# Performance work log

Hardware: AMD Instinct MI355X
Metric: run time of the kernel (lower is better)

## Reference

```python
import jax, jax.numpy as jnp
import numpy as np
import math

H = 768      # hidden_dim
NH = 12      # nhead
HD = H // NH # head_dim
FF = 4 * H
B, N = 8, 1024


def _layernorm(x, g, b, eps=1e-5):
    m = jnp.mean(x, axis=-1, keepdims=True)
    v = jnp.var(x, axis=-1, keepdims=True)
    return (x - m) * jax.lax.rsqrt(v + eps) * g + b


def setup_inputs() -> dict:
    key = jax.random.key(0)
    ks = jax.random.split(key, 16)
    s = 1.0 / math.sqrt(H)
    inp = {
        'x': jax.random.normal(ks[0], (B, N, H), jnp.float32),
        'attn_bias': jax.random.normal(ks[1], (NH, N, N), jnp.float32),
        'Wq': jax.random.normal(ks[2], (H, H), jnp.float32) * s,
        'bq': jnp.zeros((H,), jnp.float32),
        'Wk': jax.random.normal(ks[3], (H, H), jnp.float32) * s,
        'bk': jnp.zeros((H,), jnp.float32),
        'Wv': jax.random.normal(ks[4], (H, H), jnp.float32) * s,
        'bv': jnp.zeros((H,), jnp.float32),
        'Wo': jax.random.normal(ks[5], (H, H), jnp.float32) * s,
        'bo': jnp.zeros((H,), jnp.float32),
        'g1': jnp.ones((H,), jnp.float32),
        'be1': jnp.zeros((H,), jnp.float32),
        'W1': jax.random.normal(ks[6], (H, FF), jnp.float32) * s,
        'bf1': jnp.zeros((FF,), jnp.float32),
        'W2': jax.random.normal(ks[7], (FF, H), jnp.float32) * (1.0 / math.sqrt(FF)),
        'bf2': jnp.zeros((H,), jnp.float32),
        'g2': jnp.ones((H,), jnp.float32),
        'be2': jnp.zeros((H,), jnp.float32),
    }
    return inp


def reference(x, attn_bias, Wq, bq, Wk, bk, Wv, bv, Wo, bo, g1, be1, W1, bf1, W2, bf2, g2, be2):
    # dropout in eval mode (identity)
    Bc, Nc, C = x.shape
    q = (x @ Wq + bq).reshape(Bc, Nc, NH, HD).transpose(0, 2, 1, 3)  # [B,H,N,D]
    k = (x @ Wk + bk).reshape(Bc, Nc, NH, HD).transpose(0, 2, 1, 3)
    v = (x @ Wv + bv).reshape(Bc, Nc, NH, HD).transpose(0, 2, 1, 3)
    scores = jnp.einsum('bhnd,bhmd->bhnm', q, k) / math.sqrt(HD)
    scores = scores + attn_bias[None]  # bias broadcast over batch
    probs = jax.nn.softmax(scores, axis=-1)
    out = jnp.einsum('bhnm,bhmd->bhnd', probs, v)
    out = out.transpose(0, 2, 1, 3).reshape(Bc, Nc, C)
    out = out @ Wo + bo
    x = _layernorm(x + out, g1, be1)
    h = jax.nn.gelu(x @ W1 + bf1, approximate=False) @ W2 + bf2
    x = _layernorm(x + h, g2, be2)
    return x
```

## Files before the change

### kernel.cpp

```cpp
#include <hip/hip_runtime.h>
#include <math.h>

#define NH 12
#define HD 64
#define SEQ 1024
#define BATCH 8
#define HDIM 768
#define FFDIM 3072
#define MTOT (BATCH*SEQ)

typedef __attribute__((ext_vector_type(8))) short short8;
typedef __attribute__((ext_vector_type(4))) float f32x4;
typedef __attribute__((ext_vector_type(4))) unsigned short ushort4v;

__device__ __forceinline__ unsigned short f2b(float f) {
    union { float f; unsigned u; } v; v.f = f;
    unsigned r = v.u + 0x7fffu + ((v.u >> 16) & 1u);
    return (unsigned short)(r >> 16);
}

__device__ __forceinline__ f32x4 mfma16(short8 a, short8 b, f32x4 c) {
    return __builtin_amdgcn_mfma_f32_16x16x32_bf16(a, b, c, 0, 0, 0);
}

__device__ __forceinline__ void async_copy16(const unsigned short* g, unsigned short* l) {
    __builtin_amdgcn_global_load_lds(
        (const __attribute__((address_space(1))) unsigned int*)(const void*)g,
        (__attribute__((address_space(3))) unsigned int*)(void*)l, 16, 0, 0);
}

__global__ __launch_bounds__(256) void k_cvt(const float* __restrict__ in,
                                             unsigned short* __restrict__ out, int n) {
    int idx = (blockIdx.x * 256 + threadIdx.x) * 4;
    if (idx >= n) return;
    float4 v = *reinterpret_cast<const float4*>(in + idx);
    ushort4v o;
    o[0] = f2b(v.x); o[1] = f2b(v.y); o[2] = f2b(v.z); o[3] = f2b(v.w);
    *reinterpret_cast<ushort4v*>(out + idx) = o;
}

__global__ __launch_bounds__(256) void k_wt4(const float* __restrict__ W0,
                                             const float* __restrict__ W1,
                                             const float* __restrict__ W2,
                                             const float* __restrict__ W3,
                                             unsigned short* __restrict__ WT) {
    __shared__ float t[32][33];
    const float* W = (blockIdx.z == 0) ? W0 : (blockIdx.z == 1) ? W1 :
                     (blockIdx.z == 2) ? W2 : W3;
    unsigned short* dst = WT + (size_t)blockIdx.z * 768 * 768;
    int n0 = blockIdx.x * 32, k0 = blockIdx.y * 32;
    int x = threadIdx.x & 31, y = threadIdx.x >> 5;
#pragma unroll
    for (int i = y; i < 32; i += 8) t[i][x] = W[(size_t)(k0 + i) * 768 + n0 + x];
    __syncthreads();
#pragma unroll
    for (int i = y; i < 32; i += 8) dst[(size_t)(n0 + i) * 768 + k0 + x] = f2b(t[x][i]);
}

__global__ __launch_bounds__(256) void k_wt(const float* __restrict__ W,
                                            unsigned short* __restrict__ WT, int K, int Nn) {
    __shared__ float t[32][33];
    int n0 = blockIdx.x * 32, k0 = blockIdx.y * 32;
    int x = threadIdx.x & 31, y = threadIdx.x >> 5;
#pragma unroll
    for (int i = y; i < 32; i += 8) t[i][x] = W[(size_t)(k0 + i) * Nn + n0 + x];
    __syncthreads();
#pragma unroll
    for (int i = y; i < 32; i += 8) WT[(size_t)(n0 + i) * K + k0 + x] = f2b(t[x][i]);
}

__global__ void k_bias3(const float* __restrict__ a, const float* __restrict__ b,
                        const float* __restrict__ c, float* __restrict__ o) {
    int i = blockIdx.x * 256 + threadIdx.x;
    if (i >= 3 * HDIM) return;
    o[i] = (i < HDIM) ? a[i] : (i < 2 * HDIM ? b[i - HDIM] : c[i - 2 * HDIM]);
}

__global__ __launch_bounds__(256) void k_vtr(const unsigned short* __restrict__ QKV,
                                             unsigned short* __restrict__ VT) {
    __shared__ unsigned short T[64][72];
    int kt = blockIdx.x * 64;
    int bh = blockIdx.y;
    int b = bh / NH, h = bh % NH;
    int tid = threadIdx.x;
#pragma unroll
    for (int it = 0; it < 2; ++it) {
        int idx = tid + it * 256;
        int r = idx >> 3, c8 = (idx & 7) * 8;
        *reinterpret_cast<short8*>(&T[r][c8]) = *reinterpret_cast<const short8*>(
            &QKV[(size_t)(b * SEQ + kt + r) * 2304 + 1536 + h * 64 + c8]);
    }
    __syncthreads();
#pragma unroll
    for (int it = 0; it < 2; ++it) {
        int idx = tid + it * 256;
        int d = idx >> 3, c8 = (idx & 7) * 8;
        short8 o;
#pragma unroll
        for (int j = 0; j < 8; j++) {
            int slot = c8 + j;
            o[j] = (short)T[(slot & 15) * 4 + (slot >> 4)][d];
        }
        *reinterpret_cast<short8*>(&VT[((size_t)bh * 64 + d) * SEQ + kt + c8]) = o;
    }
}

template<int EPI>
__device__ __forceinline__ void epi_store(float v, size_t oi,
                                          unsigned short* outb, float* outf,
                                          const float* resid) {
    if constexpr (EPI == 0) {
        outb[oi] = f2b(v);
    } else if constexpr (EPI == 1) {
        outf[oi] = v + resid[oi];
    } else {
        float g = 0.5f * v * (1.0f + erff(v * 0.70710678118654752f));
        outb[oi] = f2b(g);
    }
}

template<int EPI>
__global__ __launch_bounds__(256) void k_gemm(const unsigned short* __restrict__ A,
                                              const unsigned short* __restrict__ BT,
                                              const float* __restrict__ bias,
                                              const float* __restrict__ resid,
                                              unsigned short* __restrict__ outb,
                                              float* __restrict__ outf,
                                              int Ndim, int Kdim) {
    __shared__ unsigned short As[128 * 64];
    __shared__ unsigned short Bs[128 * 64];
    int tid = threadIdx.x;
    int wid = tid >> 6, lane = tid & 63;
    int wm = wid >> 1, wn = wid & 1;
    int l15 = lane & 15, l16 = lane >> 4;
    int bm = blockIdx.x * 128, bn = blockIdx.y * 128;

    int srow = wid * 8 + (lane >> 3);
    int scol = 8 * ((lane & 7) ^ (lane >> 3));
    const unsigned short* aptr = A + (size_t)(bm + srow) * Kdim + scol;
    const unsigned short* bptr = BT + (size_t)(bn + srow) * Kdim + scol;

    f32x4 acc[4][4] = {};
    const int swz = (l15 & 7) << 3;

    for (int kt = 0; kt < Kdim; kt += 64) {
#pragma unroll
        for (int c = 0; c < 4; c++) {
            async_copy16(aptr + (size_t)c * 32 * Kdim + kt, As + c * 2048 + wid * 512);
            async_copy16(bptr + (size_t)c * 32 * Kdim + kt, Bs + c * 2048 + wid * 512);
        }
        __syncthreads();
#pragma unroll
        for (int kk = 0; kk < 2; kk++) {
            short8 af[4], bfr[4];
            int cidx = (kk * 32 + l16 * 8) ^ swz;
#pragma unroll
            for (int i = 0; i < 4; i++) {
                af[i]  = *reinterpret_cast<const short8*>(&As[(wm * 64 + i * 16 + l15) * 64 + cidx]);
                bfr[i] = *reinterpret_cast<const short8*>(&Bs[(wn * 64 + i * 16 + l15) * 64 + cidx]);
            }
#pragma unroll
            for (int i = 0; i < 4; i++)
#pragma unroll
                for (int j = 0; j < 4; j++)
                    acc[i][j] = mfma16(af[i], bfr[j], acc[i][j]);
        }
        __syncthreads();
    }

#pragma unroll
    for (int i = 0; i < 4; i++)
#pragma unroll
        for (int j = 0; j < 4; j++) {
            int grow0 = bm + wm * 64 + i * 16 + l16 * 4;
            int gcol = bn + wn * 64 + j * 16 + l15;
            float bcol = bias[gcol];
#pragma unroll
            for (int r = 0; r < 4; r++)
                epi_store<EPI>(acc[i][j][r] + bcol, (size_t)(grow0 + r) * Ndim + gcol,
                               outb, outf, resid);
        }
}

__global__ __launch_bounds__(256) void k_attn(const unsigned short* __restrict__ QKV,
                                              const unsigned short* __restrict__ VT,
                                              const float* __restrict__ bias,
                                              unsigned short* __restrict__ out) {
    __shared__ unsigned short Ks[64][72];
    __shared__ unsigned short Vt[64][72];
    __shared__ unsigned short Ps[4][16][72];

    int bh = blockIdx.y;
    int b = bh / NH, h = bh % NH;
    int q0 = blockIdx.x * 64;
    int tid = threadIdx.x, wid = tid >> 6, lane = tid & 63;
    int l15 = lane & 15, l16 = lane >> 4;

    size_t qrow = (size_t)(b * SEQ + q0 + wid * 16 + l15) * 2304 + h * 64;
    short8 qf0 = *reinterpret_cast<const short8*>(&QKV[qrow + l16 * 8]);
    short8 qf1 = *reinterpret_cast<const short8*>(&QKV[qrow + 32 + l16 * 8]);

    const float* brow = bias + (size_t)h * SEQ * SEQ +
                        (size_t)(q0 + wid * 16 + l16 * 4) * SEQ;

    f32x4 o[4] = {};
    float mrow[4], lrow[4];
#pragma unroll
    for (int r = 0; r < 4; r++) { mrow[r] = -1e30f; lrow[r] = 0.0f; }

    for (int kt = 0; kt < SEQ; kt += 64) {
#pragma unroll
        for (int it = 0; it < 2; ++it) {
            int idx = tid + it * 256;
            int r = idx >> 3, c8 = (idx & 7) * 8;
            int pr = (r & 15) * 4 + (r >> 4);
            *reinterpret_cast<short8*>(&Ks[r][c8]) = *reinterpret_cast<const short8*>(
                &QKV[(size_t)(b * SEQ + kt + pr) * 2304 + 768 + h * 64 + c8]);
            *reinterpret_cast<short8*>(&Vt[r][c8]) = *reinterpret_cast<const short8*>(
                &VT[((size_t)bh * 64 + r) * SEQ + kt + c8]);
        }
        __syncthreads();

        f32x4 s[4];
#pragma unroll
        for (int c = 0; c < 4; c++) {
            f32x4 t = {};
            t = mfma16(qf0, *reinterpret_cast<const short8*>(&Ks[c * 16 + l15][l16 * 8]), t);
            t = mfma16(qf1, *reinterpret_cast<const short8*>(&Ks[c * 16 + l15][32 + l16 * 8]), t);
            s[c] = t;
        }
#pragma unroll
        for (int r = 0; r < 4; r++) {
            float4 bv = *reinterpret_cast<const float4*>(&brow[(size_t)r * SEQ + kt + l15 * 4]);
            s[0][r] = s[0][r] * 0.125f + bv.x;
            s[1][r] = s[1][r] * 0.125f + bv.y;
            s[2][r] = s[2][r] * 0.125f + bv.z;
            s[3][r] = s[3][r] * 0.125f + bv.w;
        }
#pragma unroll
        for (int r = 0; r < 4; r++) {
            float mx = fmaxf(fmaxf(s[0][r], s[1][r]), fmaxf(s[2][r], s[3][r]));
#pragma unroll
            for (int off = 1; off < 16; off <<= 1) mx = fmaxf(mx, __shfl_xor(mx, off, 64));
            float mnew = fmaxf(mrow[r], mx);
            float resc = __expf(mrow[r] - mnew);
            mrow[r] = mnew;
            float sum = 0.0f;
#pragma unroll
            for (int c = 0; c < 4; c++) {
                float p = __expf(s[c][r] - mnew);
                s[c][r] = p; sum += p;
            }
#pragma unroll
            for (int off = 1; off < 16; off <<= 1) sum += __shfl_xor(sum, off, 64);
            lrow[r] = lrow[r] * resc + sum;
#pragma unroll
            for (int dc = 0; dc < 4; dc++) o[dc][r] *= resc;
        }
#pragma unroll
        for (int c = 0; c < 4; c++)
#pragma unroll
            for (int r = 0; r < 4; r++)
                Ps[wid][l16 * 4 + r][c * 16 + l15] = f2b(s[c][r]);
#pragma unroll
        for (int dc = 0; dc < 4; dc++) {
            int d = dc * 16 + l15;
#pragma unroll
            for (int kk = 0; kk < 2; kk++) {
                short8 pa = *reinterpret_cast<const short8*>(&Ps[wid][l15][kk * 32 + l16 * 8]);
                short8 vb = *reinterpret_cast<const short8*>(&Vt[d][kk * 32 + l16 * 8]);
                o[dc] = mfma16(pa, vb, o[dc]);
            }
        }
        __syncthreads();
    }

#pragma unroll
    for (int dc = 0; dc < 4; dc++)
#pragma unroll
        for (int r = 0; r < 4; r++) {
            float v = o[dc][r] / lrow[r];
            size_t row = (size_t)(b * SEQ + q0 + wid * 16 + l16 * 4 + r);
            out[row * 768 + h * 64 + dc * 16 + l15] = f2b(v);
        }
}

template<int WB>
__global__ __launch_bounds__(256) void k_ln(const float* __restrict__ in,
                                            const float* __restrict__ gw,
                                            const float* __restrict__ bw,
                                            float* __restrict__ outf,
                                            unsigned short* __restrict__ outb) {
    int row = blockIdx.x, tid = threadIdx.x;
    const float* x = in + (size_t)row * 768;
    float v0 = x[tid], v1 = x[tid + 256], v2 = x[tid + 512];
    float s = v0 + v1 + v2;
    float s2 = v0 * v0 + v1 * v1 + v2 * v2;
#pragma unroll
    for (int off = 32; off; off >>= 1) {
        s += __shfl_down(s, off, 64);
        s2 += __shfl_down(s2, off, 64);
    }
    __shared__ float red[16];
    if ((tid & 63) == 0) { red[tid >> 6] = s; red[8 + (tid >> 6)] = s2; }
    __syncthreads();
    float ssum = red[0] + red[1] + red[2] + red[3];
    float s2sum = red[8] + red[9] + red[10] + red[11];
    float mean = ssum * (1.0f / 768.0f);
    float var = s2sum * (1.0f / 768.0f) - mean * mean;
    float rstd = rsqrtf(var + 1e-5f);
    float* of = outf + (size_t)row * 768;
    unsigned short* ob = outb ? outb + (size_t)row * 768 : nullptr;
    float vv[3] = { v0, v1, v2 };
#pragma unroll
    for (int i = 0; i < 3; i++) {
        int col = tid + i * 256;
        float y = (vv[i] - mean) * rstd * gw[col] + bw[col];
        of[col] = y;
        if constexpr (WB) ob[col] = f2b(y);
    }
}

constexpr size_t OFF_XB    = 0;
constexpr size_t OFF_QKV   = OFF_XB    + 12582912;
constexpr size_t OFF_ATT   = OFF_QKV   + 37748736;
constexpr size_t OFF_WQKVT = OFF_ATT   + 12582912;
constexpr size_t OFF_WOT   = OFF_WQKVT + 3538944;
constexpr size_t OFF_W1T   = OFF_WOT   + 1179648;
constexpr size_t OFF_W2T   = OFF_W1T   + 4718592;
constexpr size_t OFF_BQKV  = OFF_W2T   + 4718592;
constexpr size_t OFF_TMP   = OFF_BQKV  + 9216;
constexpr size_t OFF_X1F   = OFF_TMP   + 25165824;
constexpr size_t OFF_X1B   = OFF_X1F   + 25165824;
constexpr size_t OFF_H     = OFF_X1B   + 12582912;

extern "C" void kernel_launch(void* const* d_in, const int* in_sizes, int n_in,
                              void* d_out, int out_size, void* d_ws, size_t ws_size,
                              hipStream_t stream) {
    const float* x    = (const float*)d_in[0];
    const float* ab   = (const float*)d_in[1];
    const float* Wq   = (const float*)d_in[2];
    const float* bq   = (const float*)d_in[3];
    const float* Wk   = (const float*)d_in[4];
    const float* bk   = (const float*)d_in[5];
    const float* Wv   = (const float*)d_in[6];
    const float* bv   = (const float*)d_in[7];
    const float* Wo   = (const float*)d_in[8];
    const float* bo   = (const float*)d_in[9];
    const float* g1   = (const float*)d_in[10];
    const float* be1  = (const float*)d_in[11];
    const float* W1   = (const float*)d_in[12];
    const float* bf1  = (const float*)d_in[13];
    const float* W2   = (const float*)d_in[14];
    const float* bf2  = (const float*)d_in[15];
    const float* g2   = (const float*)d_in[16];
    const float* be2  = (const float*)d_in[17];

    char* ws = (char*)d_ws;
    unsigned short* xb    = (unsigned short*)(ws + OFF_XB);
    unsigned short* qkv   = (unsigned short*)(ws + OFF_QKV);
    unsigned short* att   = (unsigned short*)(ws + OFF_ATT);
    unsigned short* wqkvt = (unsigned short*)(ws + OFF_WQKVT);
    unsigned short* wot   = (unsigned short*)(ws + OFF_WOT);
    unsigned short* w1t   = (unsigned short*)(ws + OFF_W1T);
    unsigned short* w2t   = (unsigned short*)(ws + OFF_W2T);
    float*          bqkv  = (float*)(ws + OFF_BQKV);
    float*          tmp   = (float*)(ws + OFF_TMP);
    unsigned short* vt    = (unsigned short*)(ws + OFF_TMP);
    float*          x1f   = (float*)(ws + OFF_X1F);
    unsigned short* x1b   = (unsigned short*)(ws + OFF_X1B);
    unsigned short* hb    = (unsigned short*)(ws + OFF_H);
    float*          out   = (float*)d_out;

    k_cvt<<<dim3(MTOT * HDIM / 1024), dim3(256), 0, stream>>>(x, xb, MTOT * HDIM);
    k_wt4<<<dim3(24, 24, 4), dim3(256), 0, stream>>>(Wq, Wk, Wv, Wo, wqkvt);
    k_wt<<<dim3(96, 24), dim3(256), 0, stream>>>(W1, w1t, HDIM, FFDIM);
    k_wt<<<dim3(24, 96), dim3(256), 0, stream>>>(W2, w2t, FFDIM, HDIM);
    k_bias3<<<dim3(9), dim3(256), 0, stream>>>(bq, bk, bv, bqkv);

    k_gemm<0><<<dim3(64, 18), dim3(256), 0, stream>>>(xb, wqkvt, bqkv, nullptr, qkv, nullptr,
                                                      3 * HDIM, HDIM);
    k_vtr<<<dim3(SEQ / 64, BATCH * NH), dim3(256), 0, stream>>>(qkv, vt);
    k_attn<<<dim3(SEQ / 64, BATCH * NH), dim3(256), 0, stream>>>(qkv, vt, ab, att);
    k_gemm<1><<<dim3(64, 6), dim3(256), 0, stream>>>(att, wot, bo, x, nullptr, tmp,
                                                     HDIM, HDIM);
    k_ln<1><<<dim3(MTOT), dim3(256), 0, stream>>>(tmp, g1, be1, x1f, x1b);
    k_gemm<2><<<dim3(64, 24), dim3(256), 0, stream>>>(x1b, w1t, bf1, nullptr, hb, nullptr,
                                                      FFDIM, HDIM);
    k_gemm<1><<<dim3(64, 6), dim3(256), 0, stream>>>(hb, w2t, bf2, x1f, nullptr, tmp,
                                                     HDIM, FFDIM);
    k_ln<0><<<dim3(MTOT), dim3(256), 0, stream>>>(tmp, g2, be2, out, nullptr);
}
```

Before: 495.5 us.

## Transpose attention score tiles and use lazy online-softmax rescaling

Swaps the MFMA operand order so each lane owns one query row of the score tile. This reduces the row max and sum reductions to two cross-group shuffles and lets K and V be loaded without the row permutation. The 1/sqrt(d) scale is folded into the Wq weights and bias during preprocessing. Online-softmax rescaling is skipped while the running max grows by at most 8. Probabilities are packed to bf16 with v_cvt_pk_bf16 and stored as vectors, and an extra block barrier is added inside the loop.

Result: slower. 517.4 us (+4.4%).

```diff
diff --git a/kernel.cpp b/kernel.cpp
--- a/kernel.cpp
+++ b/kernel.cpp
@@ -17,6 +17,12 @@
     union { float f; unsigned u; } v; v.f = f;
     unsigned r = v.u + 0x7fffu + ((v.u >> 16) & 1u);
     return (unsigned short)(r >> 16);
+}
+
+__device__ __forceinline__ unsigned cvt_pk_bf16(float lo, float hi) {
+    unsigned r;
+    asm("v_cvt_pk_bf16_f32 %0, %1, %2" : "=v"(r) : "v"(lo), "v"(hi));
+    return r;
 }
 
 __device__ __forceinline__ f32x4 mfma16(short8 a, short8 b, f32x4 c) {
@@ -47,6 +53,7 @@
     __shared__ float t[32][33];
     const float* W = (blockIdx.z == 0) ? W0 : (blockIdx.z == 1) ? W1 :
                      (blockIdx.z == 2) ? W2 : W3;
+    float sc = (blockIdx.z == 0) ? 0.125f : 1.0f;
     unsigned short* dst = WT + (size_t)blockIdx.z * 768 * 768;
     int n0 = blockIdx.x * 32, k0 = blockIdx.y * 32;
     int x = threadIdx.x & 31, y = threadIdx.x >> 5;
@@ -54,7 +61,7 @@
     for (int i = y; i < 32; i += 8) t[i][x] = W[(size_t)(k0 + i) * 768 + n0 + x];
     __syncthreads();
 #pragma unroll
-    for (int i = y; i < 32; i += 8) dst[(size_t)(n0 + i) * 768 + k0 + x] = f2b(t[x][i]);
+    for (int i = y; i < 32; i += 8) dst[(size_t)(n0 + i) * 768 + k0 + x] = f2b(t[x][i] * sc);
 }
 
 __global__ __launch_bounds__(256) void k_wt(const float* __restrict__ W,
@@ -73,7 +80,7 @@
                         const float* __restrict__ c, float* __restrict__ o) {
     int i = blockIdx.x * 256 + threadIdx.x;
     if (i >= 3 * HDIM) return;
-    o[i] = (i < HDIM) ? a[i] : (i < 2 * HDIM ? b[i - HDIM] : c[i - 2 * HDIM]);
+    o[i] = (i < HDIM) ? a[i] * 0.125f : (i < 2 * HDIM ? b[i - HDIM] : c[i - 2 * HDIM]);
 }
 
 __global__ __launch_bounds__(256) void k_vtr(const unsigned short* __restrict__ QKV,
@@ -97,10 +104,7 @@
         int d = idx >> 3, c8 = (idx & 7) * 8;
         short8 o;
 #pragma unroll
-        for (int j = 0; j < 8; j++) {
-            int slot = c8 + j;
-            o[j] = (short)T[(slot & 15) * 4 + (slot >> 4)][d];
-        }
+        for (int j = 0; j < 8; j++) o[j] = (short)T[c8 + j][d];
         *reinterpret_cast<short8*>(&VT[((size_t)bh * 64 + d) * SEQ + kt + c8]) = o;
     }
 }
@@ -200,22 +204,18 @@
     short8 qf0 = *reinterpret_cast<const short8*>(&QKV[qrow + l16 * 8]);
     short8 qf1 = *reinterpret_cast<const short8*>(&QKV[qrow + 32 + l16 * 8]);
 
-    const float* brow = bias + (size_t)h * SEQ * SEQ +
-                        (size_t)(q0 + wid * 16 + l16 * 4) * SEQ;
+    const float* brow = bias + (size_t)h * SEQ * SEQ + (size_t)(q0 + wid * 16 + l15) * SEQ;
 
     f32x4 o[4] = {};
-    float mrow[4], lrow[4];
-#pragma unroll
-    for (int r = 0; r < 4; r++) { mrow[r] = -1e30f; lrow[r] = 0.0f; }
+    float mrow = -1e30f, lrow = 0.0f;
 
     for (int kt = 0; kt < SEQ; kt += 64) {
 #pragma unroll
         for (int it = 0; it < 2; ++it) {
             int idx = tid + it * 256;
             int r = idx >> 3, c8 = (idx & 7) * 8;
-            int pr = (r & 15) * 4 + (r >> 4);
             *reinterpret_cast<short8*>(&Ks[r][c8]) = *reinterpret_cast<const short8*>(
-                &QKV[(size_t)(b * SEQ + kt + pr) * 2304 + 768 + h * 64 + c8]);
+                &QKV[(size_t)(b * SEQ + kt + r) * 2304 + 768 + h * 64 + c8]);
             *reinterpret_cast<short8*>(&Vt[r][c8]) = *reinterpret_cast<const short8*>(
                 &VT[((size_t)bh * 64 + r) * SEQ + kt + c8]);
         }
@@ -225,43 +225,52 @@
 #pragma unroll
         for (int c = 0; c < 4; c++) {
             f32x4 t = {};
-            t = mfma16(qf0, *reinterpret_cast<const short8*>(&Ks[c * 16 + l15][l16 * 8]), t);
-            t = mfma16(qf1, *reinterpret_cast<const short8*>(&Ks[c * 16 + l15][32 + l16 * 8]), t);
+            t = mfma16(*reinterpret_cast<const short8*>(&Ks[c * 16 + l15][l16 * 8]), qf0, t);
+            t = mfma16(*reinterpret_cast<const short8*>(&Ks[c * 16 + l15][32 + l16 * 8]), qf1, t);
             s[c] = t;
         }
 #pragma unroll
-        for (int r = 0; r < 4; r++) {
-            float4 bv = *reinterpret_cast<const float4*>(&brow[(size_t)r * SEQ + kt + l15 * 4]);
-            s[0][r] = s[0][r] * 0.125f + bv.x;
-            s[1][r] = s[1][r] * 0.125f + bv.y;
-            s[2][r] = s[2][r] * 0.125f + bv.z;
-            s[3][r] = s[3][r] * 0.125f + bv.w;
-        }
-#pragma unroll
-        for (int r = 0; r < 4; r++) {
-            float mx = fmaxf(fmaxf(s[0][r], s[1][r]), fmaxf(s[2][r], s[3][r]));
-#pragma unroll
-            for (int off = 1; off < 16; off <<= 1) mx = fmaxf(mx, __shfl_xor(mx, off, 64));
-            float mnew = fmaxf(mrow[r], mx);
-            float resc = __expf(mrow[r] - mnew);
-            mrow[r] = mnew;
-            float sum = 0.0f;
-#pragma unroll
-            for (int c = 0; c < 4; c++) {
-                float p = __expf(s[c][r] - mnew);
-                s[c][r] = p; sum += p;
+        for (int c = 0; c < 4; c++) {
+            float4 bv = *reinterpret_cast<const float4*>(&brow[kt + c * 16 + l16 * 4]);
+            s[c][0] += bv.x; s[c][1] += bv.y; s[c][2] += bv.z; s[c][3] += bv.w;
+        }
+        float pmax = fmaxf(fmaxf(fmaxf(s[0][0], s[0][1]), fmaxf(s[0][2], s[0][3])),
+                           fmaxf(fmaxf(s[1][0], s[1][1]), fmaxf(s[1][2], s[1][3])));
+        pmax = fmaxf(pmax, fmaxf(fmaxf(fmaxf(s[2][0], s[2][1]), fmaxf(s[2][2], s[2][3])),
+                                 fmaxf(fmaxf(s[3][0], s[3][1]), fmaxf(s[3][2], s[3][3]))));
+        pmax = fmaxf(pmax, __shfl_xor(pmax, 16, 64));
+        pmax = fmaxf(pmax, __shfl_xor(pmax, 32, 64));
+        if (!__all(pmax - mrow <= 8.0f)) {
+            float mnew = fmaxf(mrow, pmax);
+            float resc = __expf(mrow - mnew);
+            mrow = mnew;
+            lrow *= resc;
+#pragma unroll
+            for (int r = 0; r < 4; r++) {
+                float rb = __shfl(resc, l16 * 4 + r, 16);
+#pragma unroll
+                for (int dc = 0; dc < 4; dc++) o[dc][r] *= rb;
             }
-#pragma unroll
-            for (int off = 1; off < 16; off <<= 1) sum += __shfl_xor(sum, off, 64);
-            lrow[r] = lrow[r] * resc + sum;
-#pragma unroll
-            for (int dc = 0; dc < 4; dc++) o[dc][r] *= resc;
-        }
+        }
+        float psum = 0.0f;
 #pragma unroll
         for (int c = 0; c < 4; c++)
 #pragma unroll
-            for (int r = 0; r < 4; r++)
-                Ps[wid][l16 * 4 + r][c * 16 + l15] = f2b(s[c][r]);
+            for (int r = 0; r < 4; r++) {
+                float p = __expf(s[c][r] - mrow);
+                s[c][r] = p; psum += p;
+            }
+        psum += __shfl_xor(psum, 16, 64);
+        psum += __shfl_xor(psum, 32, 64);
+        lrow += psum;
+#pragma unroll
+        for (int c = 0; c < 4; c++) {
+            uint2 pk;
+            pk.x = cvt_pk_bf16(s[c][0], s[c][1]);
+            pk.y = cvt_pk_bf16(s[c][2], s[c][3]);
+            *reinterpret_cast<uint2*>(&Ps[wid][l15][c * 16 + l16 * 4]) = pk;
+        }
+        __syncthreads();
 #pragma unroll
         for (int dc = 0; dc < 4; dc++) {
             int d = dc * 16 + l15;
@@ -276,13 +285,14 @@
     }
 
 #pragma unroll
-    for (int dc = 0; dc < 4; dc++)
-#pragma unroll
-        for (int r = 0; r < 4; r++) {
-            float v = o[dc][r] / lrow[r];
-            size_t row = (size_t)(b * SEQ + q0 + wid * 16 + l16 * 4 + r);
-            out[row * 768 + h * 64 + dc * 16 + l15] = f2b(v);
-        }
+    for (int r = 0; r < 4; r++) {
+        float lb = __shfl(lrow, l16 * 4 + r, 16);
+        float linv = 1.0f / lb;
+        size_t row = (size_t)(b * SEQ + q0 + wid * 16 + l16 * 4 + r);
+#pragma unroll
+        for (int dc = 0; dc < 4; dc++)
+            out[row * 768 + h * 64 + dc * 16 + l15] = f2b(o[dc][r] * linv);
+    }
 }
 
 template<int WB>
```
